# Kernel optimization log

Hardware: AMD Instinct MI355X
Metric: run time of the kernel (lower is better)

## Reference

```python
import jax, jax.numpy as jnp
import numpy as np

P = 32    # num_particles
B = 64    # batch_size
T = 100   # seq_len
W = 50    # window_length
E = 64    # act embedding dim (emb_obs=0)
H = 256   # hidden_dim
ALPHA = 0.5  # resamp_alpha


def setup_inputs() -> dict:
    key = jax.random.key(0)
    ks = jax.random.split(key, 12)
    def lin(k, fan_in, shape):
        return jax.random.normal(k, shape, jnp.float32) / np.sqrt(fan_in).astype(np.float32)
    u = jax.random.uniform(ks[4], (T, B, P, P), jnp.float32, 1e-6, 1.0 - 1e-6)
    return {
        "prev_window": jax.random.normal(ks[0], (B, T, W), jnp.float32),
        "h0": jax.random.uniform(ks[1], (P * B, H), jnp.float32),
        "c0": jax.random.uniform(ks[2], (P * B, H), jnp.float32),
        "eps": jax.random.normal(ks[3], (T, P * B, H), jnp.float32),
        "gumbel": -jnp.log(-jnp.log(u)),  # Gumbel noise for multinomial resampling
        "W_act": lin(ks[5], W, (W, E)), "b_act": jnp.zeros((E,), jnp.float32),
        "W_ih": lin(ks[6], E, (E, 5 * H)), "b_ih": jnp.zeros((5 * H,), jnp.float32),
        "W_hh": lin(ks[7], H, (H, 5 * H)), "b_hh": jnp.zeros((5 * H,), jnp.float32),
        "W_obs": lin(ks[8], H + E, (H + E, 1)), "b_obs": jnp.zeros((1,), jnp.float32),
        "W_lab": lin(ks[9], H, (H, 1)), "b_lab": jnp.zeros((1,), jnp.float32),
    }


def reference(prev_window, h0, c0, eps, gumbel, W_act, b_act, W_ih, b_ih,
              W_hh, b_hh, W_obs, b_obs, W_lab, b_lab):
    # act embedding, tiled over particles (particle-major, matching torch repeat)
    emb = jax.nn.relu(prev_window @ W_act + b_act)          # [B,T,E]
    xs = jnp.swapaxes(jnp.tile(emb, (P, 1, 1)), 0, 1)       # [T,P*B,E]
    p0 = jnp.full((P * B, 1), np.log(1.0 / P), jnp.float32)

    barange = jnp.arange(B)

    def step(carry, inputs):
        h, c, p = carry                                      # [PB,H],[PB,H],[PB,1]
        x, eps_t, g_t = inputs                               # [PB,E],[PB,H],[B,P,P]
        gates = x @ W_ih + b_ih + h @ W_hh + b_hh            # [PB,5H]
        i, f, g, o, var = jnp.split(gates, 5, axis=1)
        mu = jax.nn.sigmoid(f) * c + jax.nn.sigmoid(i) * jnp.tanh(g)
        c1 = mu + jax.nn.softplus(var) * eps_t               # stochastic cell (reparameterize)
        h1 = jax.nn.sigmoid(o) * jnp.tanh(c1)
        # observation log-likelihood per particle
        logpdf = jnp.concatenate([h1, x], axis=1) @ W_obs + b_obs  # [PB,1]
        p1 = jax.nn.log_softmax((p + logpdf).reshape(P, B), axis=0)  # [P,B]
        # soft resampling: q = alpha*w + (1-alpha)/P, sample via Gumbel-argmax
        w1 = jnp.exp(p1)
        logits = jnp.log(ALPHA * w1 + (1.0 - ALPHA) / P)     # [P_src,B]
        idx = jnp.argmax(logits.T[:, None, :] + g_t, axis=-1).T  # [P_new,B]
        h_new = h1.reshape(P, B, H)[idx, barange[None, :]]   # [P,B,H]
        c_new = c1.reshape(P, B, H)[idx, barange[None, :]]
        w = w1[idx, barange[None, :]]                        # [P,B]
        w = w / (ALPHA * w + (1.0 - ALPHA) / P)              # importance correction
        p_new = jax.nn.log_softmax(jnp.log(w), axis=0)
        h_new = h_new.reshape(P * B, H)
        c_new = c_new.reshape(P * B, H)
        p_new = p_new.reshape(P * B, 1)
        return (h_new, c_new, p_new), (h_new, p_new)

    _, (hs, ps) = jax.lax.scan(step, (h0, c0, p0), (xs, eps, gumbel))
    # hs: [T,PB,H], ps: [T,PB,1]; dropout rate 0 -> identity
    prob = ps.reshape(T, P, B, 1)
    out = hs.reshape(T, P, B, H)
    y = jnp.sum(out * jnp.exp(prob), axis=1)                 # weighted particle mean [T,B,H]
    y_out = jax.nn.sigmoid(y @ W_lab + b_lab)                # [T,B,1]
    pf_out = jax.nn.sigmoid(hs @ W_lab + b_lab)              # [T,PB,1]
    return y_out, pf_out
```

## Files before the change

### kernel.cpp

```cpp
#include <hip/hip_runtime.h>
#include <hip/hip_bf16.h>
#include <cstddef>
#include <cstdint>

#define PP 32
#define BB 64
#define TT 100
#define WW 50
#define EE 64
#define HH 256

typedef float f4 __attribute__((ext_vector_type(4)));
typedef __attribute__((ext_vector_type(8))) short short8;
typedef __attribute__((ext_vector_type(4))) float f32x4;

__device__ __forceinline__ float sigm(float x) { return 1.0f / (1.0f + expf(-x)); }
__device__ __forceinline__ float splus(float x) {
    return fmaxf(x, 0.0f) + log1pf(expf(-fabsf(x)));
}
__device__ __forceinline__ unsigned short bfh(float x) {
    __hip_bfloat16 h = __float2bfloat16(x);
    return *reinterpret_cast<unsigned short*>(&h);
}
__device__ __forceinline__ float bff(unsigned short u) {
    __hip_bfloat16 h; *reinterpret_cast<unsigned short*>(&h) = u;
    return __bfloat162float(h);
}

__global__ __launch_bounds__(256) void k_emb(
    const float* __restrict__ pw, const float* __restrict__ w_act,
    const float* __restrict__ b_act, const float* __restrict__ w_obs,
    const float* __restrict__ b_obs,
    float* __restrict__ emb, float* __restrict__ xobs)
{
    int tid = threadIdx.x;
    int sub = tid >> 6;
    int e   = tid & 63;
    int bt  = blockIdx.x * 4 + sub;
    int b = bt / TT, t = bt % TT;

    __shared__ float pws[4][WW + 2];
    if (e < WW) pws[sub][e] = pw[(size_t)bt * WW + e];
    __syncthreads();

    float acc = b_act[e];
    #pragma unroll 5
    for (int w = 0; w < WW; ++w) acc += pws[sub][w] * w_act[w * EE + e];
    float r = fmaxf(acc, 0.0f);
    emb[((size_t)t * BB + b) * EE + e] = r;

    float xv = r * w_obs[HH + e];
    #pragma unroll
    for (int d = 1; d < 64; d <<= 1) xv += __shfl_xor(xv, d);
    if (e == 0) xobs[t * BB + b] = xv + b_obs[0];
}

__global__ __launch_bounds__(256) void k_embW(
    const float* __restrict__ emb, const float* __restrict__ W_ih,
    float* __restrict__ embW)
{
    int t  = blockIdx.x / 16;
    int cp = blockIdx.x - (blockIdx.x / 16) * 16;
    int tid = threadIdx.x;

    __shared__ float le[64][65];
    __shared__ float lw[64][80];

    {
        const f4* src = (const f4*)(emb + (size_t)t * 4096);
        for (int i = tid; i < 1024; i += 256) {
            f4 v = src[i];
            int b = i >> 4, e0 = (i & 15) * 4;
            le[b][e0 + 0] = v.x; le[b][e0 + 1] = v.y;
            le[b][e0 + 2] = v.z; le[b][e0 + 3] = v.w;
        }
    }
    {
        for (int i = tid; i < 5120; i += 256) {
            int e = i / 80, c = i - e * 80;
            int g = c >> 4, lh = c & 15;
            lw[e][c] = W_ih[(size_t)e * 1280 + g * 256 + cp * 16 + lh];
        }
    }
    __syncthreads();

    int lh = tid & 15, bq = tid >> 4;
    #pragma unroll
    for (int g = 0; g < 5; ++g) {
        float a0 = 0, a1 = 0, a2 = 0, a3 = 0;
        #pragma unroll
        for (int e = 0; e < 64; ++e) {
            float wv = lw[e][g * 16 + lh];
            a0 += le[bq * 4 + 0][e] * wv;
            a1 += le[bq * 4 + 1][e] * wv;
            a2 += le[bq * 4 + 2][e] * wv;
            a3 += le[bq * 4 + 3][e] * wv;
        }
        f4 o = {a0, a1, a2, a3};
        *(f4*)&embW[(((size_t)t * 16 + cp) * 5 + g) * 1024 + lh * 64 + bq * 4] = o;
    }
}

__global__ __launch_bounds__(256) void k_packB(
    const float* __restrict__ W_ih, const float* __restrict__ W_hh,
    unsigned short* __restrict__ Bp)
{
    int i = blockIdx.x * 256 + threadIdx.x;
    int colp = i / 51200;  int r = i - colp * 51200;
    int bidx = r / 2560;   r -= bidx * 2560;
    int g    = r / 512;    r -= g * 512;
    int lane = r >> 3;     int e = r & 7;

    int c = (bidx < 10) ? bidx : (bidx - 10);
    int k = c * 32 + (lane >> 4) * 8 + e;
    int col = g * HH + colp * 16 + (lane & 15);
    float w = (k < HH) ? W_hh[(size_t)k * 1280 + col]
                       : W_ih[(size_t)(k - HH) * 1280 + col];
    unsigned short uh = bfh(w);
    Bp[i] = (bidx < 10) ? uh : bfh(w - bff(uh));
}

__global__ __launch_bounds__(256) void k_split0(
    const float* __restrict__ h0, const float* __restrict__ c0,
    unsigned short* __restrict__ hh, unsigned short* __restrict__ hl,
    float* __restrict__ cc)
{
    int i = blockIdx.x * 256 + threadIdx.x;
    float v = h0[i];
    unsigned short uh = bfh(v);
    hh[i] = uh;
    hl[i] = bfh(v - bff(uh));
    cc[i] = c0[i];
}

__global__ __launch_bounds__(256, 2) void s1_mfma(
    const unsigned short* __restrict__ Bp,
    const float* __restrict__ embW_t,
    const unsigned short* __restrict__ hh_in, const unsigned short* __restrict__ hl_in,
    const float* __restrict__ c_in,
    unsigned short* __restrict__ hh_out, unsigned short* __restrict__ hl_out,
    float* __restrict__ c_out,
    const int* __restrict__ gidx,
    const float* __restrict__ b_ih, const float* __restrict__ b_hh,
    const float* __restrict__ w_obs, const float* __restrict__ w_lab,
    const float* __restrict__ eps_t,
    float* __restrict__ dpo, float* __restrict__ dpl)
{
    __shared__ short8 BhL[2560];

    const int tid  = threadIdx.x;
    const int rp   = blockIdx.x & 31;
    const int cp   = blockIdx.x >> 5;
    const int lane = tid & 63;
    const int w    = tid >> 6;
    const int lh   = lane & 15;
    const int kq   = lane >> 4;
    const int R0   = rp * 64 + w * 16;

    {
        const short8* src = (const short8*)Bp + (size_t)cp * 6400;
        for (int s = tid; s < 2560; s += 256) BhL[s] = src[s];
    }

    const int myrow = R0 + lh;
    const int sr    = gidx ? gidx[myrow] : myrow;
    const size_t hoff = (size_t)sr * 512 + (size_t)kq * 16;

    f32x4 acc[5];
    #pragma unroll
    for (int g = 0; g < 5; ++g) acc[g] = (f32x4)(0.0f);

    const char* hhp = (const char*)hh_in + hoff;
    const char* hlp = (const char*)hl_in + hoff;
    const short8* bslab = (const short8*)Bp + (size_t)cp * 6400 + lane;

    __syncthreads();

    #pragma unroll
    for (int cs = 0; cs < 8; ++cs) {
        short8 Ah = *(const short8*)(hhp + cs * 64);
        short8 Al = *(const short8*)(hlp + cs * 64);
        short8 Bh[5], Bl[5];
        #pragma unroll
        for (int g = 0; g < 5; ++g) {
            Bh[g] = BhL[(cs * 5 + g) * 64 + lane];
            Bl[g] = bslab[((cs + 10) * 5 + g) * 64];
        }
        #pragma unroll
        for (int g = 0; g < 5; ++g)
            acc[g] = __builtin_amdgcn_mfma_f32_16x16x32_bf16(Ah, Bh[g], acc[g], 0, 0, 0);
        #pragma unroll
        for (int g = 0; g < 5; ++g)
            acc[g] = __builtin_amdgcn_mfma_f32_16x16x32_bf16(Ah, Bl[g], acc[g], 0, 0, 0);
        #pragma unroll
        for (int g = 0; g < 5; ++g)
            acc[g] = __builtin_amdgcn_mfma_f32_16x16x32_bf16(Al, Bh[g], acc[g], 0, 0, 0);
    }

    const int hcol = cp * 16 + lh;
    float bsum[5];
    #pragma unroll
    for (int g = 0; g < 5; ++g) bsum[g] = b_ih[g * HH + hcol] + b_hh[g * HH + hcol];
    const float wobs_l = w_obs[hcol];
    const float wlab_l = w_lab[hcol];

    f4 ew[5];
    #pragma unroll
    for (int g = 0; g < 5; ++g)
        ew[g] = *(const f4*)&embW_t[((size_t)cp * 5 + g) * 1024 + lh * 64 + w * 16 + kq * 4];

    #pragma unroll
    for (int reg = 0; reg < 4; ++reg) {
        int row = R0 + kq * 4 + reg;
        int sr2 = gidx ? gidx[row] : row;
        float cpv = c_in[(size_t)sr2 * HH + hcol];
        float ep  = eps_t[(size_t)row * HH + hcol];

        float gi = acc[0][reg] + bsum[0] + ew[0][reg];
        float gf = acc[1][reg] + bsum[1] + ew[1][reg];
        float gg = acc[2][reg] + bsum[2] + ew[2][reg];
        float go = acc[3][reg] + bsum[3] + ew[3][reg];
        float gv = acc[4][reg] + bsum[4] + ew[4][reg];

        float mu  = sigm(gf) * cpv + sigm(gi) * tanhf(gg);
        float c1v = mu + splus(gv) * ep;
        float h1v = sigm(go) * tanhf(c1v);

        c_out[(size_t)row * HH + hcol] = c1v;
        unsigned short uh = bfh(h1v);
        hh_out[(size_t)row * HH + hcol] = uh;
        hl_out[(size_t)row * HH + hcol] = bfh(h1v - bff(uh));

        float po = h1v * wobs_l, pl = h1v * wlab_l;
        po += __shfl_xor(po, 1); po += __shfl_xor(po, 2);
        po += __shfl_xor(po, 4); po += __shfl_xor(po, 8);
        pl += __shfl_xor(pl, 1); pl += __shfl_xor(pl, 2);
        pl += __shfl_xor(pl, 4); pl += __shfl_xor(pl, 8);
        if (lh == 0) {
            dpo[cp * 2048 + row] = po;
            dpl[cp * 2048 + row] = pl;
        }
    }
}

__global__ __launch_bounds__(256) void s2_kernel(
    const float* __restrict__ dpo, const float* __restrict__ dpl,
    const float* __restrict__ xobs_t, const float* __restrict__ g_t,
    const float* __restrict__ b_lab,
    float* __restrict__ p_buf, int first,
    int* __restrict__ gidx_next,
    float* __restrict__ y_out_t, float* __restrict__ pf_out_t)
{
    int b   = blockIdx.x;
    int tid = threadIdx.x;

    __shared__ float gt[PP][PP + 1];
    __shared__ float lg[PP];
    __shared__ float w1s[PP];
    __shared__ float lgt[PP];
    __shared__ float pnew[PP];
    __shared__ float dpart[PP];
    __shared__ int   idxs[PP];

    {
        f4 v = ((const f4*)(g_t + (size_t)b * 1024))[tid];
        int p = tid >> 3, j0 = (tid & 7) * 4;
        gt[p][j0 + 0] = v.x; gt[p][j0 + 1] = v.y;
        gt[p][j0 + 2] = v.z; gt[p][j0 + 3] = v.w;
    }

    int p = tid >> 3, j = tid & 7;
    {
        int o = p * BB + b;
        float s = dpo[j * 2048 + o] + dpo[(j + 8) * 2048 + o];
        s += __shfl_xor(s, 1); s += __shfl_xor(s, 2); s += __shfl_xor(s, 4);
        if (j == 0) {
            float pprev = first ? -3.4657359027997265f : p_buf[o];
            lg[p] = pprev + s + xobs_t[b];
        }
    }
    __syncthreads();

    if (tid < 32) {
        float v = lg[tid];
        float m = v;
        #pragma unroll
        for (int d = 1; d < 32; d <<= 1) m = fmaxf(m, __shfl_xor(m, d));
        float e = expf(v - m), se = e;
        #pragma unroll
        for (int d = 1; d < 32; d <<= 1) se += __shfl_xor(se, d);
        float l1 = v - m - logf(se);
        float w1 = expf(l1);
        w1s[tid] = w1;
        lgt[tid] = logf(0.5f * w1 + 0.015625f);
    }
    __syncthreads();

    if (tid < 32) {
        int p2 = tid;
        float best = -INFINITY; int bi = 0;
        #pragma unroll 8
        for (int jj = 0; jj < 32; ++jj) {
            float val = lgt[jj] + gt[p2][jj];
            if (val > best) { best = val; bi = jj; }
        }
        idxs[p2] = bi;
        gidx_next[p2 * BB + b] = bi * BB + b;

        float wv = w1s[bi];
        wv = wv / (0.5f * wv + 0.015625f);
        float lw = logf(wv);
        float m2 = lw;
        #pragma unroll
        for (int d = 1; d < 32; d <<= 1) m2 = fmaxf(m2, __shfl_xor(m2, d));
        float e2 = expf(lw - m2), s2 = e2;
        #pragma unroll
        for (int d = 1; d < 32; d <<= 1) s2 += __shfl_xor(s2, d);
        float pn = lw - m2 - logf(s2);
        pnew[p2] = pn;
        p_buf[p2 * BB + b] = pn;
    }
    __syncthreads();

    {
        int src = idxs[p] * BB + b;
        float d = dpl[j * 2048 + src] + dpl[(j + 8) * 2048 + src];
        d += __shfl_xor(d, 1); d += __shfl_xor(d, 2); d += __shfl_xor(d, 4);
        if (j == 0) dpart[p] = d;
    }
    __syncthreads();

    if (tid < 32) {
        float dd = dpart[tid];
        float bl = b_lab[0];
        pf_out_t[tid * BB + b] = 1.0f / (1.0f + expf(-(dd + bl)));
        float contrib = expf(pnew[tid]) * dd;
        #pragma unroll
        for (int d = 1; d < 32; d <<= 1) contrib += __shfl_xor(contrib, d);
        if (tid == 0) y_out_t[b] = 1.0f / (1.0f + expf(-(contrib + bl)));
    }
}

extern "C" void kernel_launch(void* const* d_in, const int* in_sizes, int n_in,
                              void* d_out, int out_size, void* d_ws, size_t ws_size,
                              hipStream_t stream)
{
    const float* prev_window = (const float*)d_in[0];
    const float* h0    = (const float*)d_in[1];
    const float* c0    = (const float*)d_in[2];
    const float* eps   = (const float*)d_in[3];
    const float* gum   = (const float*)d_in[4];
    const float* W_act = (const float*)d_in[5];
    const float* b_act = (const float*)d_in[6];
    const float* W_ih  = (const float*)d_in[7];
    const float* b_ih  = (const float*)d_in[8];
    const float* W_hh  = (const float*)d_in[9];
    const float* b_hh  = (const float*)d_in[10];
    const float* W_obs = (const float*)d_in[11];
    const float* b_obs = (const float*)d_in[12];
    const float* W_lab = (const float*)d_in[13];
    const float* b_lab = (const float*)d_in[14];

    float* out = (float*)d_out;
    char* w = (char*)d_ws;

    unsigned short* Bp   = (unsigned short*)(w);
    float*  emb  = (float*)(w + 1638400);
    float*  embW = (float*)(w + 3276800);
    unsigned short* hhA  = (unsigned short*)(w + 36044800);
    unsigned short* hlA  = (unsigned short*)(w + 37093376);
    unsigned short* hhB  = (unsigned short*)(w + 38141952);
    unsigned short* hlB  = (unsigned short*)(w + 39190528);
    float*  cA   = (float*)(w + 40239104);
    float*  cB   = (float*)(w + 42336256);
    float*  xobs = (float*)(w + 44433408);
    float*  pbuf = (float*)(w + 44459008);
    int*    gidx = (int*)(w + 44467200);
    float*  dpo  = (float*)(w + 44475392);
    float*  dpl  = (float*)(w + 44606464);

    k_emb<<<1600, 256, 0, stream>>>(prev_window, W_act, b_act, W_obs, b_obs,
                                    emb, xobs);
    k_embW<<<1600, 256, 0, stream>>>(emb, W_ih, embW);
    k_packB<<<3200, 256, 0, stream>>>(W_ih, W_hh, Bp);
    k_split0<<<2048, 256, 0, stream>>>(h0, c0, hhA, hlA, cA);

    for (int t = 0; t < TT; ++t) {
        const unsigned short* hh_in = (t & 1) ? hhB : hhA;
        const unsigned short* hl_in = (t & 1) ? hlB : hlA;
        const float*          c_in  = (t & 1) ? cB  : cA;
        unsigned short* hh_out = (t & 1) ? hhA : hhB;
        unsigned short* hl_out = (t & 1) ? hlA : hlB;
        float*          c_out  = (t & 1) ? cA  : cB;

        s1_mfma<<<512, 256, 0, stream>>>(
            Bp, embW + (size_t)t * 81920,
            hh_in, hl_in, c_in, hh_out, hl_out, c_out,
            (t == 0) ? nullptr : gidx,
            b_ih, b_hh, W_obs, W_lab,
            eps + (size_t)t * 524288,
            dpo, dpl);

        s2_kernel<<<64, 256, 0, stream>>>(
            dpo, dpl, xobs + t * BB, gum + (size_t)t * 65536,
            b_lab, pbuf, (t == 0) ? 1 : 0, gidx,
            out + (size_t)t * BB,
            out + (size_t)TT * BB + (size_t)t * PP * BB);
    }
}
```

Measured before the change: 2.449 ms.

## Fuse whole particle-filter recurrence into one persistent per-batch kernel with LDS state

Replaces the 200 per-timestep launches (an MFMA gate kernel plus a resampling kernel) with a single persistent kernel. It runs one 512-thread block per batch element and loops over all timesteps. The h (split into hi/lo bf16) and c state stay in shared memory, and resampling indices are applied as an indirection into LDS rows instead of gathering from global buffers. The input projection is precomputed in a row-major layout, and the packed weights now cover only W_hh. This removes launch overhead and global round trips of the state. The cost is that only 64 blocks are active, and each one re-reads the full packed weight matrix from cache every step.

```diff
diff --git a/kernel.cpp b/kernel.cpp
--- a/kernel.cpp
+++ b/kernel.cpp
@@ -11,6 +11,7 @@
 #define HH 256
 
 typedef float f4 __attribute__((ext_vector_type(4)));
+typedef float f2 __attribute__((ext_vector_type(2)));
 typedef __attribute__((ext_vector_type(8))) short short8;
 typedef __attribute__((ext_vector_type(4))) float f32x4;
 
@@ -57,10 +58,10 @@
 
 __global__ __launch_bounds__(256) void k_embW(
     const float* __restrict__ emb, const float* __restrict__ W_ih,
-    float* __restrict__ embW)
+    float* __restrict__ embW2)
 {
     int t  = blockIdx.x / 16;
-    int cp = blockIdx.x - (blockIdx.x / 16) * 16;
+    int cp = blockIdx.x - t * 16;
     int tid = threadIdx.x;
 
     __shared__ float le[64][65];
@@ -74,8 +75,6 @@
             le[b][e0 + 0] = v.x; le[b][e0 + 1] = v.y;
             le[b][e0 + 2] = v.z; le[b][e0 + 3] = v.w;
         }
-    }
-    {
         for (int i = tid; i < 5120; i += 256) {
             int e = i / 80, c = i - e * 80;
             int g = c >> 4, lh = c & 15;
@@ -96,248 +95,245 @@
             a2 += le[bq * 4 + 2][e] * wv;
             a3 += le[bq * 4 + 3][e] * wv;
         }
-        f4 o = {a0, a1, a2, a3};
-        *(f4*)&embW[(((size_t)t * 16 + cp) * 5 + g) * 1024 + lh * 64 + bq * 4] = o;
-    }
-}
-
-__global__ __launch_bounds__(256) void k_packB(
-    const float* __restrict__ W_ih, const float* __restrict__ W_hh,
-    unsigned short* __restrict__ Bp)
+        size_t base = ((size_t)t * 64) * 1280 + g * 256 + cp * 16 + lh;
+        embW2[base + (size_t)(bq * 4 + 0) * 1280] = a0;
+        embW2[base + (size_t)(bq * 4 + 1) * 1280] = a1;
+        embW2[base + (size_t)(bq * 4 + 2) * 1280] = a2;
+        embW2[base + (size_t)(bq * 4 + 3) * 1280] = a3;
+    }
+}
+
+__global__ __launch_bounds__(256) void k_packBk(
+    const float* __restrict__ W_hh, unsigned short* __restrict__ Bpk)
 {
     int i = blockIdx.x * 256 + threadIdx.x;
-    int colp = i / 51200;  int r = i - colp * 51200;
-    int bidx = r / 2560;   r -= bidx * 2560;
-    int g    = r / 512;    r -= g * 512;
-    int lane = r >> 3;     int e = r & 7;
-
-    int c = (bidx < 10) ? bidx : (bidx - 10);
-    int k = c * 32 + (lane >> 4) * 8 + e;
-    int col = g * HH + colp * 16 + (lane & 15);
-    float w = (k < HH) ? W_hh[(size_t)k * 1280 + col]
-                       : W_ih[(size_t)(k - HH) * 1280 + col];
-    unsigned short uh = bfh(w);
-    Bp[i] = (bidx < 10) ? uh : bfh(w - bff(uh));
-}
-
-__global__ __launch_bounds__(256) void k_split0(
+    int e    = i & 7;
+    int lane = (i >> 3) & 63;
+    int ci   = (i >> 9) & 15;
+    int fgh  = i >> 13;
+    int g  = fgh % 5, hf = fgh / 5;
+    int cs = ci & 7;
+    int k   = cs * 32 + (lane >> 4) * 8 + e;
+    int col = g * 256 + hf * 16 + (lane & 15);
+    float wv = W_hh[(size_t)k * 1280 + col];
+    unsigned short uh = bfh(wv);
+    Bpk[i] = (ci < 8) ? uh : bfh(wv - bff(uh));
+}
+
+__global__ __launch_bounds__(512, 2) void pf_all(
+    const unsigned short* __restrict__ Bpk,
+    const float* __restrict__ embW2,
     const float* __restrict__ h0, const float* __restrict__ c0,
-    unsigned short* __restrict__ hh, unsigned short* __restrict__ hl,
-    float* __restrict__ cc)
-{
-    int i = blockIdx.x * 256 + threadIdx.x;
-    float v = h0[i];
-    unsigned short uh = bfh(v);
-    hh[i] = uh;
-    hl[i] = bfh(v - bff(uh));
-    cc[i] = c0[i];
-}
-
-__global__ __launch_bounds__(256, 2) void s1_mfma(
-    const unsigned short* __restrict__ Bp,
-    const float* __restrict__ embW_t,
-    const unsigned short* __restrict__ hh_in, const unsigned short* __restrict__ hl_in,
-    const float* __restrict__ c_in,
-    unsigned short* __restrict__ hh_out, unsigned short* __restrict__ hl_out,
-    float* __restrict__ c_out,
-    const int* __restrict__ gidx,
+    const float* __restrict__ eps, const float* __restrict__ gumG,
+    const float* __restrict__ xobs,
     const float* __restrict__ b_ih, const float* __restrict__ b_hh,
-    const float* __restrict__ w_obs, const float* __restrict__ w_lab,
-    const float* __restrict__ eps_t,
-    float* __restrict__ dpo, float* __restrict__ dpl)
-{
-    __shared__ short8 BhL[2560];
+    const float* __restrict__ W_obs, const float* __restrict__ W_lab,
+    const float* __restrict__ b_lab,
+    float* __restrict__ y_out, float* __restrict__ pf_out)
+{
+    __shared__ unsigned short hhS[32 * 264];
+    __shared__ unsigned short hlS[32 * 264];
+    __shared__ float cS[32 * 264];
+    __shared__ float gumS[32][33];
+    __shared__ float wdp[8][32][2];
+    __shared__ float w1S[32], lgtS[32], dlS[32], pbS[32];
+    __shared__ int   idxS[32];
 
     const int tid  = threadIdx.x;
-    const int rp   = blockIdx.x & 31;
-    const int cp   = blockIdx.x >> 5;
+    const int b    = blockIdx.x;
+    const int w    = tid >> 6;
     const int lane = tid & 63;
-    const int w    = tid >> 6;
     const int lh   = lane & 15;
     const int kq   = lane >> 4;
-    const int R0   = rp * 64 + w * 16;
-
-    {
-        const short8* src = (const short8*)Bp + (size_t)cp * 6400;
-        for (int s = tid; s < 2560; s += 256) BhL[s] = src[s];
-    }
-
-    const int myrow = R0 + lh;
-    const int sr    = gidx ? gidx[myrow] : myrow;
-    const size_t hoff = (size_t)sr * 512 + (size_t)kq * 16;
-
-    f32x4 acc[5];
+
+    for (int s = tid; s < 8192; s += 512) {
+        int p = s >> 8, k = s & 255;
+        float v = h0[((size_t)p * 64 + b) * 256 + k];
+        unsigned short uh = bfh(v);
+        hhS[p * 264 + k] = uh;
+        hlS[p * 264 + k] = bfh(v - bff(uh));
+        cS [p * 264 + k] = c0[((size_t)p * 64 + b) * 256 + k];
+    }
+    if (tid < 32) { idxS[tid] = tid; pbS[tid] = -3.4657359027997265f; }
+
+    const int hcA = (2 * w) * 16 + lh;
+    const int hcB = hcA + 16;
+    float bsum[5][2];
     #pragma unroll
-    for (int g = 0; g < 5; ++g) acc[g] = (f32x4)(0.0f);
-
-    const char* hhp = (const char*)hh_in + hoff;
-    const char* hlp = (const char*)hl_in + hoff;
-    const short8* bslab = (const short8*)Bp + (size_t)cp * 6400 + lane;
+    for (int g = 0; g < 5; ++g) {
+        bsum[g][0] = b_ih[g * 256 + hcA] + b_hh[g * 256 + hcA];
+        bsum[g][1] = b_ih[g * 256 + hcB] + b_hh[g * 256 + hcB];
+    }
+    const float wobs0 = W_obs[hcA], wobs1 = W_obs[hcB];
+    const float wlab0 = W_lab[hcA], wlab1 = W_lab[hcB];
+    const float blab  = b_lab[0];
+    const short8* bsl = (const short8*)Bpk;
 
     __syncthreads();
 
-    #pragma unroll
-    for (int cs = 0; cs < 8; ++cs) {
-        short8 Ah = *(const short8*)(hhp + cs * 64);
-        short8 Al = *(const short8*)(hlp + cs * 64);
-        short8 Bh[5], Bl[5];
-        #pragma unroll
-        for (int g = 0; g < 5; ++g) {
-            Bh[g] = BhL[(cs * 5 + g) * 64 + lane];
-            Bl[g] = bslab[((cs + 10) * 5 + g) * 64];
-        }
+    for (int t = 0; t < TT; ++t) {
+        {
+            const f2* gp = (const f2*)(gumG + (size_t)t * 65536 + (size_t)b * 1024);
+            f2 v = gp[tid];
+            int p = tid >> 4, j0 = (tid & 15) * 2;
+            gumS[p][j0] = v.x; gumS[p][j0 + 1] = v.y;
+        }
+        const int rA0 = idxS[lh];
+        const int rA1 = idxS[16 + lh];
+        float ew[5][2];
+        {
+            const float* ewb = embW2 + ((size_t)t * 64 + b) * 1280;
+            #pragma unroll
+            for (int g = 0; g < 5; ++g) {
+                ew[g][0] = ewb[g * 256 + hcA];
+                ew[g][1] = ewb[g * 256 + hcB];
+            }
+        }
+        float cpre[2][2][4], epre[2][2][4];
+        #pragma unroll
+        for (int fr = 0; fr < 2; ++fr)
+            #pragma unroll
+            for (int reg = 0; reg < 4; ++reg) {
+                int row = fr * 16 + kq * 4 + reg;
+                int ar  = idxS[row];
+                cpre[0][fr][reg] = cS[ar * 264 + hcA];
+                cpre[1][fr][reg] = cS[ar * 264 + hcB];
+                const float* ep = eps + ((size_t)t * 2048 + (size_t)row * 64 + b) * 256;
+                epre[0][fr][reg] = ep[hcA];
+                epre[1][fr][reg] = ep[hcB];
+            }
+
+        f32x4 acc[5][2][2];
         #pragma unroll
         for (int g = 0; g < 5; ++g)
-            acc[g] = __builtin_amdgcn_mfma_f32_16x16x32_bf16(Ah, Bh[g], acc[g], 0, 0, 0);
-        #pragma unroll
-        for (int g = 0; g < 5; ++g)
-            acc[g] = __builtin_amdgcn_mfma_f32_16x16x32_bf16(Ah, Bl[g], acc[g], 0, 0, 0);
-        #pragma unroll
-        for (int g = 0; g < 5; ++g)
-            acc[g] = __builtin_amdgcn_mfma_f32_16x16x32_bf16(Al, Bh[g], acc[g], 0, 0, 0);
-    }
-
-    const int hcol = cp * 16 + lh;
-    float bsum[5];
-    #pragma unroll
-    for (int g = 0; g < 5; ++g) bsum[g] = b_ih[g * HH + hcol] + b_hh[g * HH + hcol];
-    const float wobs_l = w_obs[hcol];
-    const float wlab_l = w_lab[hcol];
-
-    f4 ew[5];
-    #pragma unroll
-    for (int g = 0; g < 5; ++g)
-        ew[g] = *(const f4*)&embW_t[((size_t)cp * 5 + g) * 1024 + lh * 64 + w * 16 + kq * 4];
-
-    #pragma unroll
-    for (int reg = 0; reg < 4; ++reg) {
-        int row = R0 + kq * 4 + reg;
-        int sr2 = gidx ? gidx[row] : row;
-        float cpv = c_in[(size_t)sr2 * HH + hcol];
-        float ep  = eps_t[(size_t)row * HH + hcol];
-
-        float gi = acc[0][reg] + bsum[0] + ew[0][reg];
-        float gf = acc[1][reg] + bsum[1] + ew[1][reg];
-        float gg = acc[2][reg] + bsum[2] + ew[2][reg];
-        float go = acc[3][reg] + bsum[3] + ew[3][reg];
-        float gv = acc[4][reg] + bsum[4] + ew[4][reg];
-
-        float mu  = sigm(gf) * cpv + sigm(gi) * tanhf(gg);
-        float c1v = mu + splus(gv) * ep;
-        float h1v = sigm(go) * tanhf(c1v);
-
-        c_out[(size_t)row * HH + hcol] = c1v;
-        unsigned short uh = bfh(h1v);
-        hh_out[(size_t)row * HH + hcol] = uh;
-        hl_out[(size_t)row * HH + hcol] = bfh(h1v - bff(uh));
-
-        float po = h1v * wobs_l, pl = h1v * wlab_l;
-        po += __shfl_xor(po, 1); po += __shfl_xor(po, 2);
-        po += __shfl_xor(po, 4); po += __shfl_xor(po, 8);
-        pl += __shfl_xor(pl, 1); pl += __shfl_xor(pl, 2);
-        pl += __shfl_xor(pl, 4); pl += __shfl_xor(pl, 8);
-        if (lh == 0) {
-            dpo[cp * 2048 + row] = po;
-            dpl[cp * 2048 + row] = pl;
-        }
-    }
-}
-
-__global__ __launch_bounds__(256) void s2_kernel(
-    const float* __restrict__ dpo, const float* __restrict__ dpl,
-    const float* __restrict__ xobs_t, const float* __restrict__ g_t,
-    const float* __restrict__ b_lab,
-    float* __restrict__ p_buf, int first,
-    int* __restrict__ gidx_next,
-    float* __restrict__ y_out_t, float* __restrict__ pf_out_t)
-{
-    int b   = blockIdx.x;
-    int tid = threadIdx.x;
-
-    __shared__ float gt[PP][PP + 1];
-    __shared__ float lg[PP];
-    __shared__ float w1s[PP];
-    __shared__ float lgt[PP];
-    __shared__ float pnew[PP];
-    __shared__ float dpart[PP];
-    __shared__ int   idxs[PP];
-
-    {
-        f4 v = ((const f4*)(g_t + (size_t)b * 1024))[tid];
-        int p = tid >> 3, j0 = (tid & 7) * 4;
-        gt[p][j0 + 0] = v.x; gt[p][j0 + 1] = v.y;
-        gt[p][j0 + 2] = v.z; gt[p][j0 + 3] = v.w;
-    }
-
-    int p = tid >> 3, j = tid & 7;
-    {
-        int o = p * BB + b;
-        float s = dpo[j * 2048 + o] + dpo[(j + 8) * 2048 + o];
-        s += __shfl_xor(s, 1); s += __shfl_xor(s, 2); s += __shfl_xor(s, 4);
-        if (j == 0) {
-            float pprev = first ? -3.4657359027997265f : p_buf[o];
-            lg[p] = pprev + s + xobs_t[b];
-        }
-    }
-    __syncthreads();
-
-    if (tid < 32) {
-        float v = lg[tid];
-        float m = v;
-        #pragma unroll
-        for (int d = 1; d < 32; d <<= 1) m = fmaxf(m, __shfl_xor(m, d));
-        float e = expf(v - m), se = e;
-        #pragma unroll
-        for (int d = 1; d < 32; d <<= 1) se += __shfl_xor(se, d);
-        float l1 = v - m - logf(se);
-        float w1 = expf(l1);
-        w1s[tid] = w1;
-        lgt[tid] = logf(0.5f * w1 + 0.015625f);
-    }
-    __syncthreads();
-
-    if (tid < 32) {
-        int p2 = tid;
-        float best = -INFINITY; int bi = 0;
-        #pragma unroll 8
-        for (int jj = 0; jj < 32; ++jj) {
-            float val = lgt[jj] + gt[p2][jj];
-            if (val > best) { best = val; bi = jj; }
-        }
-        idxs[p2] = bi;
-        gidx_next[p2 * BB + b] = bi * BB + b;
-
-        float wv = w1s[bi];
-        wv = wv / (0.5f * wv + 0.015625f);
-        float lw = logf(wv);
-        float m2 = lw;
-        #pragma unroll
-        for (int d = 1; d < 32; d <<= 1) m2 = fmaxf(m2, __shfl_xor(m2, d));
-        float e2 = expf(lw - m2), s2 = e2;
-        #pragma unroll
-        for (int d = 1; d < 32; d <<= 1) s2 += __shfl_xor(s2, d);
-        float pn = lw - m2 - logf(s2);
-        pnew[p2] = pn;
-        p_buf[p2 * BB + b] = pn;
-    }
-    __syncthreads();
-
-    {
-        int src = idxs[p] * BB + b;
-        float d = dpl[j * 2048 + src] + dpl[(j + 8) * 2048 + src];
-        d += __shfl_xor(d, 1); d += __shfl_xor(d, 2); d += __shfl_xor(d, 4);
-        if (j == 0) dpart[p] = d;
-    }
-    __syncthreads();
-
-    if (tid < 32) {
-        float dd = dpart[tid];
-        float bl = b_lab[0];
-        pf_out_t[tid * BB + b] = 1.0f / (1.0f + expf(-(dd + bl)));
-        float contrib = expf(pnew[tid]) * dd;
-        #pragma unroll
-        for (int d = 1; d < 32; d <<= 1) contrib += __shfl_xor(contrib, d);
-        if (tid == 0) y_out_t[b] = 1.0f / (1.0f + expf(-(contrib + bl)));
+            #pragma unroll
+            for (int ha = 0; ha < 2; ++ha)
+                #pragma unroll
+                for (int fr = 0; fr < 2; ++fr) acc[g][ha][fr] = (f32x4)(0.0f);
+
+        #pragma unroll
+        for (int cs = 0; cs < 8; ++cs) {
+            short8 Ah0 = *(const short8*)&hhS[rA0 * 264 + cs * 32 + kq * 8];
+            short8 Ah1 = *(const short8*)&hhS[rA1 * 264 + cs * 32 + kq * 8];
+            short8 Al0 = *(const short8*)&hlS[rA0 * 264 + cs * 32 + kq * 8];
+            short8 Al1 = *(const short8*)&hlS[rA1 * 264 + cs * 32 + kq * 8];
+            #pragma unroll
+            for (int ha = 0; ha < 2; ++ha) {
+                #pragma unroll
+                for (int g = 0; g < 5; ++g) {
+                    int f = ((2 * w + ha) * 5 + g) * 16 + cs;
+                    short8 Bh = bsl[(size_t)f * 64 + lane];
+                    short8 Bl = bsl[(size_t)(f + 8) * 64 + lane];
+                    acc[g][ha][0] = __builtin_amdgcn_mfma_f32_16x16x32_bf16(Ah0, Bh, acc[g][ha][0], 0, 0, 0);
+                    acc[g][ha][0] = __builtin_amdgcn_mfma_f32_16x16x32_bf16(Ah0, Bl, acc[g][ha][0], 0, 0, 0);
+                    acc[g][ha][0] = __builtin_amdgcn_mfma_f32_16x16x32_bf16(Al0, Bh, acc[g][ha][0], 0, 0, 0);
+                    acc[g][ha][1] = __builtin_amdgcn_mfma_f32_16x16x32_bf16(Ah1, Bh, acc[g][ha][1], 0, 0, 0);
+                    acc[g][ha][1] = __builtin_amdgcn_mfma_f32_16x16x32_bf16(Ah1, Bl, acc[g][ha][1], 0, 0, 0);
+                    acc[g][ha][1] = __builtin_amdgcn_mfma_f32_16x16x32_bf16(Al1, Bh, acc[g][ha][1], 0, 0, 0);
+                }
+            }
+        }
+        __syncthreads();
+
+        float po[2][4], pl[2][4];
+        #pragma unroll
+        for (int fr = 0; fr < 2; ++fr)
+            #pragma unroll
+            for (int reg = 0; reg < 4; ++reg) { po[fr][reg] = 0.0f; pl[fr][reg] = 0.0f; }
+
+        #pragma unroll
+        for (int ha = 0; ha < 2; ++ha) {
+            int hc = ha ? hcB : hcA;
+            float wo = ha ? wobs1 : wobs0;
+            float wl = ha ? wlab1 : wlab0;
+            #pragma unroll
+            for (int fr = 0; fr < 2; ++fr)
+                #pragma unroll
+                for (int reg = 0; reg < 4; ++reg) {
+                    int row = fr * 16 + kq * 4 + reg;
+                    float gi = acc[0][ha][fr][reg] + bsum[0][ha] + ew[0][ha];
+                    float gf = acc[1][ha][fr][reg] + bsum[1][ha] + ew[1][ha];
+                    float gg = acc[2][ha][fr][reg] + bsum[2][ha] + ew[2][ha];
+                    float go = acc[3][ha][fr][reg] + bsum[3][ha] + ew[3][ha];
+                    float gv = acc[4][ha][fr][reg] + bsum[4][ha] + ew[4][ha];
+
+                    float mu  = sigm(gf) * cpre[ha][fr][reg] + sigm(gi) * tanhf(gg);
+                    float c1v = mu + splus(gv) * epre[ha][fr][reg];
+                    float h1v = sigm(go) * tanhf(c1v);
+
+                    cS[row * 264 + hc] = c1v;
+                    unsigned short uh = bfh(h1v);
+                    hhS[row * 264 + hc] = uh;
+                    hlS[row * 264 + hc] = bfh(h1v - bff(uh));
+
+                    po[fr][reg] += h1v * wo;
+                    pl[fr][reg] += h1v * wl;
+                }
+        }
+        #pragma unroll
+        for (int fr = 0; fr < 2; ++fr)
+            #pragma unroll
+            for (int reg = 0; reg < 4; ++reg) {
+                float s = po[fr][reg];
+                s += __shfl_xor(s, 1); s += __shfl_xor(s, 2);
+                s += __shfl_xor(s, 4); s += __shfl_xor(s, 8);
+                float s2 = pl[fr][reg];
+                s2 += __shfl_xor(s2, 1); s2 += __shfl_xor(s2, 2);
+                s2 += __shfl_xor(s2, 4); s2 += __shfl_xor(s2, 8);
+                if (lh == 0) {
+                    int row = fr * 16 + kq * 4 + reg;
+                    wdp[w][row][0] = s;
+                    wdp[w][row][1] = s2;
+                }
+            }
+        __syncthreads();
+
+        if (tid < 32) {
+            int p = tid;
+            float so = 0.0f, sl = 0.0f;
+            #pragma unroll
+            for (int ww = 0; ww < 8; ++ww) { so += wdp[ww][p][0]; sl += wdp[ww][p][1]; }
+            dlS[p] = sl;
+            float v = pbS[p] + so + xobs[t * 64 + b];
+            float m = v;
+            #pragma unroll
+            for (int d = 1; d < 32; d <<= 1) m = fmaxf(m, __shfl_xor(m, d));
+            float e = expf(v - m), se = e;
+            #pragma unroll
+            for (int d = 1; d < 32; d <<= 1) se += __shfl_xor(se, d);
+            float w1 = expf(v - m - logf(se));
+            w1S[p]  = w1;
+            lgtS[p] = logf(0.5f * w1 + 0.015625f);
+        }
+        __syncthreads();
+        if (tid < 32) {
+            int p = tid;
+            float best = -INFINITY; int bi = 0;
+            #pragma unroll 8
+            for (int j = 0; j < 32; ++j) {
+                float val = lgtS[j] + gumS[p][j];
+                if (val > best) { best = val; bi = j; }
+            }
+            idxS[p] = bi;
+            float wv = w1S[bi];
+            wv = wv / (0.5f * wv + 0.015625f);
+            float lw = logf(wv);
+            float m2 = lw;
+            #pragma unroll
+            for (int d = 1; d < 32; d <<= 1) m2 = fmaxf(m2, __shfl_xor(m2, d));
+            float e2 = expf(lw - m2), ss = e2;
+            #pragma unroll
+            for (int d = 1; d < 32; d <<= 1) ss += __shfl_xor(ss, d);
+            float pn = lw - m2 - logf(ss);
+            pbS[p] = pn;
+            float dd = dlS[bi];
+            pf_out[(size_t)t * 2048 + p * 64 + b] = 1.0f / (1.0f + expf(-(dd + blab)));
+            float contrib = expf(pn) * dd;
+            #pragma unroll
+            for (int d = 1; d < 32; d <<= 1) contrib += __shfl_xor(contrib, d);
+            if (p == 0) y_out[t * 64 + b] = 1.0f / (1.0f + expf(-(contrib + blab)));
+        }
+        __syncthreads();
     }
 }
 
@@ -364,47 +360,18 @@
     float* out = (float*)d_out;
     char* w = (char*)d_ws;
 
-    unsigned short* Bp   = (unsigned short*)(w);
-    float*  emb  = (float*)(w + 1638400);
-    float*  embW = (float*)(w + 3276800);
-    unsigned short* hhA  = (unsigned short*)(w + 36044800);
-    unsigned short* hlA  = (unsigned short*)(w + 37093376);
-    unsigned short* hhB  = (unsigned short*)(w + 38141952);
-    unsigned short* hlB  = (unsigned short*)(w + 39190528);
-    float*  cA   = (float*)(w + 40239104);
-    float*  cB   = (float*)(w + 42336256);
-    float*  xobs = (float*)(w + 44433408);
-    float*  pbuf = (float*)(w + 44459008);
-    int*    gidx = (int*)(w + 44467200);
-    float*  dpo  = (float*)(w + 44475392);
-    float*  dpl  = (float*)(w + 44606464);
+    unsigned short* Bpk  = (unsigned short*)(w);
+    float* emb   = (float*)(w + 1310720);
+    float* embW2 = (float*)(w + 2949120);
+    float* xobs  = (float*)(w + 35717120);
 
     k_emb<<<1600, 256, 0, stream>>>(prev_window, W_act, b_act, W_obs, b_obs,
                                     emb, xobs);
-    k_embW<<<1600, 256, 0, stream>>>(emb, W_ih, embW);
-    k_packB<<<3200, 256, 0, stream>>>(W_ih, W_hh, Bp);
-    k_split0<<<2048, 256, 0, stream>>>(h0, c0, hhA, hlA, cA);
-
-    for (int t = 0; t < TT; ++t) {
-        const unsigned short* hh_in = (t & 1) ? hhB : hhA;
-        const unsigned short* hl_in = (t & 1) ? hlB : hlA;
-        const float*          c_in  = (t & 1) ? cB  : cA;
-        unsigned short* hh_out = (t & 1) ? hhA : hhB;
-        unsigned short* hl_out = (t & 1) ? hlA : hlB;
-        float*          c_out  = (t & 1) ? cA  : cB;
-
-        s1_mfma<<<512, 256, 0, stream>>>(
-            Bp, embW + (size_t)t * 81920,
-            hh_in, hl_in, c_in, hh_out, hl_out, c_out,
-            (t == 0) ? nullptr : gidx,
-            b_ih, b_hh, W_obs, W_lab,
-            eps + (size_t)t * 524288,
-            dpo, dpl);
-
-        s2_kernel<<<64, 256, 0, stream>>>(
-            dpo, dpl, xobs + t * BB, gum + (size_t)t * 65536,
-            b_lab, pbuf, (t == 0) ? 1 : 0, gidx,
-            out + (size_t)t * BB,
-            out + (size_t)TT * BB + (size_t)t * PP * BB);
-    }
-}
+    k_embW<<<1600, 256, 0, stream>>>(emb, W_ih, embW2);
+    k_packBk<<<2560, 256, 0, stream>>>(W_hh, Bpk);
+
+    pf_all<<<64, 512, 0, stream>>>(
+        Bpk, embW2, h0, c0, eps, gum, xobs,
+        b_ih, b_hh, W_obs, W_lab, b_lab,
+        out, out + TT * BB);
+}
```

New measurement: 7.004 ms. 2.86x slower.
